# Kernel optimization log

Hardware: AMD Instinct MI355X
Metric: run time of the kernel (lower is better)

## Reference

```python
import jax, jax.numpy as jnp
import numpy as np

N = 50000
E = 1600000
IN_CH = 128
OUT_CH = 128
NEG_SLOPE = 0.2


def _gat_conv(x, W, att_src, att_dst, bias, src, dst, heads, out_ch, concat):
    # x: [N, F_in], W: [F_in, heads*out_ch], att_*: [heads, out_ch]
    n = x.shape[0]
    h = (x @ W).reshape(n, heads, out_ch)                    # [N, H, C]
    a_src = jnp.einsum('nhc,hc->nh', h, att_src)             # [N, H]
    a_dst = jnp.einsum('nhc,hc->nh', h, att_dst)             # [N, H]
    logits = jax.nn.leaky_relu(a_src[src] + a_dst[dst], NEG_SLOPE)  # [Etot, H]
    m = jax.ops.segment_max(logits, dst, num_segments=n)     # per-dst max (self-loops ensure non-empty)
    e = jnp.exp(logits - m[dst])
    denom = jax.ops.segment_sum(e, dst, num_segments=n)
    alpha = e / denom[dst]                                   # [Etot, H]
    msgs = h[src] * alpha[:, :, None]                        # [Etot, H, C]
    out = jax.ops.segment_sum(msgs, dst, num_segments=n)     # [N, H, C]
    out = out.reshape(n, heads * out_ch) if concat else out.mean(axis=1)
    return out + bias


def setup_inputs() -> dict:
    key = jax.random.key(0)
    ks = jax.random.split(key, 12)
    x = jax.random.normal(ks[0], (N, IN_CH), dtype=jnp.float32)
    edge_index = jax.random.randint(ks[1], (2, E), 0, N, dtype=jnp.int32)
    s = 0.1
    W_map = jax.random.normal(ks[2], (IN_CH, OUT_CH), dtype=jnp.float32) * s
    b_map = jnp.zeros((OUT_CH,), dtype=jnp.float32)
    # conv1: 128 -> 8 per head, 8 heads
    W1 = jax.random.normal(ks[3], (OUT_CH, 64), dtype=jnp.float32) * s
    att_src1 = jax.random.normal(ks[4], (8, 8), dtype=jnp.float32) * s
    att_dst1 = jax.random.normal(ks[5], (8, 8), dtype=jnp.float32) * s
    b1 = jnp.zeros((64,), dtype=jnp.float32)
    # conv2: 64 -> 128, 1 head, concat=False
    W2 = jax.random.normal(ks[6], (64, OUT_CH), dtype=jnp.float32) * s
    att_src2 = jax.random.normal(ks[7], (1, OUT_CH), dtype=jnp.float32) * s
    att_dst2 = jax.random.normal(ks[8], (1, OUT_CH), dtype=jnp.float32) * s
    b2 = jnp.zeros((OUT_CH,), dtype=jnp.float32)
    return {"x": x, "edge_index": edge_index, "W_map": W_map, "b_map": b_map,
            "W1": W1, "att_src1": att_src1, "att_dst1": att_dst1, "b1": b1,
            "W2": W2, "att_src2": att_src2, "att_dst2": att_dst2, "b2": b2}


def reference(x, edge_index, W_map, b_map, W1, att_src1, att_dst1, b1,
              W2, att_src2, att_dst2, b2):
    # add self-loops (PyG GATConv default)
    loops = jnp.arange(N, dtype=edge_index.dtype)
    src = jnp.concatenate([edge_index[0], loops])
    dst = jnp.concatenate([edge_index[1], loops])
    h = x @ W_map + b_map                                   # feature_mapping (dropout inactive in eval)
    h = _gat_conv(h, W1, att_src1, att_dst1, b1, src, dst, heads=8, out_ch=8, concat=True)
    h = jax.nn.elu(h)
    out = _gat_conv(h, W2, att_src2, att_dst2, b2, src, dst, heads=1, out_ch=OUT_CH, concat=False)
    return out
```

## Files before the change

### kernel.cpp

```cpp
#include <hip/hip_runtime.h>
#include <cstdint>
#include <cstddef>

#define NEG_SLOPE 0.2f
#define NBIN_MAX 1024
#define CAP_T 2560

typedef __attribute__((ext_vector_type(8))) short bf16x8;
typedef __attribute__((ext_vector_type(4))) float f32x4;

__device__ __forceinline__ float leaky(float x) { return x > 0.f ? x : NEG_SLOPE * x; }
__device__ __forceinline__ float blo(unsigned u) { return __uint_as_float(u << 16); }
__device__ __forceinline__ float bhi(unsigned u) { return __uint_as_float(u & 0xffff0000u); }
__device__ __forceinline__ unsigned short f2b(float f) {
    unsigned b = __float_as_uint(f);
    return (unsigned short)((b + 0x7fffu + ((b >> 16) & 1u)) >> 16);
}

__global__ void zero_i32(int* p, int n) {
    int i = blockIdx.x * 256 + threadIdx.x;
    if (i < n) p[i] = 0;
}

__global__ void prep_kernel(const float* __restrict__ Wm, const float* __restrict__ W1,
                            const float* __restrict__ bm, const float* __restrict__ W2,
                            unsigned short* __restrict__ WcT, float* __restrict__ bc,
                            unsigned short* __restrict__ W2T) {
    int t = blockIdx.x * 256 + threadIdx.x;
    if (t < 8192) {
        int n = t >> 7, k = t & 127;
        float acc = 0.f;
        for (int c = 0; c < 128; c++) acc = fmaf(Wm[k * 128 + c], W1[c * 64 + n], acc);
        WcT[n * 128 + k] = f2b(acc);
        if (t < 64) {
            float a = 0.f;
            for (int c = 0; c < 128; c++) a = fmaf(bm[c], W1[c * 64 + t], a);
            bc[t] = a;
        }
    } else if (t < 16384) {
        int u = t - 8192;
        int n = u >> 6, k = u & 63;
        W2T[n * 64 + k] = f2b(W2[k * 128 + n]);
    }
}

__global__ __launch_bounds__(256) void gemm1_mfma(
    const float* __restrict__ x, const unsigned short* __restrict__ WcT,
    const float* __restrict__ bc, unsigned short* __restrict__ h1b, int N) {
    int wave = threadIdx.x >> 6, l = threadIdx.x & 63;
    int mtile = blockIdx.x * 4 + wave;
    int mtiles = N >> 4;
    if (mtile >= mtiles) return;
    int lm = l & 15, quad = l >> 4;
    const float* xr = x + ((size_t)(mtile * 16 + lm)) * 128 + quad * 8;
    f32x4 acc[4];
#pragma unroll
    for (int nt = 0; nt < 4; nt++) acc[nt] = (f32x4){0.f, 0.f, 0.f, 0.f};
#pragma unroll
    for (int kk = 0; kk < 4; kk++) {
        float4 xa = ((const float4*)(xr + kk * 32))[0];
        float4 xb = ((const float4*)(xr + kk * 32 + 4))[0];
        bf16x8 a;
        a[0] = (short)f2b(xa.x); a[1] = (short)f2b(xa.y);
        a[2] = (short)f2b(xa.z); a[3] = (short)f2b(xa.w);
        a[4] = (short)f2b(xb.x); a[5] = (short)f2b(xb.y);
        a[6] = (short)f2b(xb.z); a[7] = (short)f2b(xb.w);
#pragma unroll
        for (int nt = 0; nt < 4; nt++) {
            bf16x8 b = *(const bf16x8*)(WcT + (nt * 16 + lm) * 128 + kk * 32 + quad * 8);
            acc[nt] = __builtin_amdgcn_mfma_f32_16x16x32_bf16(a, b, acc[nt], 0, 0, 0);
        }
    }
#pragma unroll
    for (int nt = 0; nt < 4; nt++) {
#pragma unroll
        for (int r = 0; r < 4; r++) {
            int row = mtile * 16 + quad * 4 + r;
            int col = nt * 16 + lm;
            h1b[(size_t)row * 64 + col] = f2b(acc[nt][r] + bc[col]);
        }
    }
}

__global__ __launch_bounds__(256) void att1_kernel(
    const unsigned* __restrict__ h1b, const float* __restrict__ att_s,
    const float* __restrict__ att_d, float* __restrict__ as1, float* __restrict__ ad1, int N) {
    __shared__ float ss[64], sd[64];
    if (threadIdx.x < 64) { ss[threadIdx.x] = att_s[threadIdx.x]; sd[threadIdx.x] = att_d[threadIdx.x]; }
    __syncthreads();
    int row = blockIdx.x * 256 + threadIdx.x;
    if (row >= N) return;
    const unsigned* hr = h1b + (size_t)row * 32;
#pragma unroll
    for (int h = 0; h < 8; h++) {
        float vs = 0.f, vd = 0.f;
#pragma unroll
        for (int cc = 0; cc < 4; cc++) {
            unsigned u = hr[h * 4 + cc];
            float lo = blo(u), hi = bhi(u);
            vs += lo * ss[h * 8 + 2 * cc] + hi * ss[h * 8 + 2 * cc + 1];
            vd += lo * sd[h * 8 + 2 * cc] + hi * sd[h * 8 + 2 * cc + 1];
        }
        as1[row * 8 + h] = vs;
        ad1[row * 8 + h] = vd;
    }
}

__global__ __launch_bounds__(256) void scatter2_kernel(
    const int* __restrict__ src, const int* __restrict__ dst, int E, int nbin,
    int* __restrict__ ccur, unsigned* __restrict__ tmp) {
    __shared__ int cnt[NBIN_MAX];
    for (int i = threadIdx.x; i < nbin; i += 256) cnt[i] = 0;
    __syncthreads();
    int chunk = (E + gridDim.x - 1) / gridDim.x;
    int beg = blockIdx.x * chunk;
    int end = beg + chunk; if (end > E) end = E;
    for (int i = beg + threadIdx.x; i < end; i += 256)
        atomicAdd(&cnt[dst[i] >> 6], 1);
    __syncthreads();
    for (int i = threadIdx.x; i < nbin; i += 256) {
        int c = cnt[i];
        cnt[i] = c ? atomicAdd(&ccur[i], c) : 0;
    }
    __syncthreads();
    for (int i = beg + threadIdx.x; i < end; i += 256) {
        int d = dst[i];
        int bin = d >> 6;
        int p = atomicAdd(&cnt[bin], 1);
        if (p < CAP_T)
            tmp[(size_t)bin * CAP_T + p] = ((unsigned)src[i] << 6) | (unsigned)(d & 63);
    }
}

__global__ __launch_bounds__(256) void bin_finalize(
    const unsigned* __restrict__ tmp, const int* __restrict__ ccur,
    int* __restrict__ off, int* __restrict__ degv,
    unsigned short* __restrict__ bucket, int N) {
    __shared__ int cnt[64];
    __shared__ int cur[64];
    int tid = threadIdx.x, b = blockIdx.x;
    if (tid < 64) cnt[tid] = 0;
    __syncthreads();
    int ecnt = ccur[b]; if (ecnt > CAP_T) ecnt = CAP_T;
    const unsigned* t = tmp + (size_t)b * CAP_T;
    for (int i = tid; i < ecnt; i += 256)
        atomicAdd(&cnt[t[i] & 63u], 1);
    __syncthreads();
    if (tid < 64) {
        int v = cnt[tid];
        int incl = v;
#pragma unroll
        for (int s = 1; s < 64; s <<= 1) {
            int u = __shfl_up(incl, s);
            if (tid >= s) incl += u;
        }
        int base = b * CAP_T + (incl - v);
        int node = b * 64 + tid;
        if (node < N) { off[node] = base; degv[node] = v; }
        cur[tid] = base;
    }
    __syncthreads();
    for (int i = tid; i < ecnt; i += 256) {
        unsigned u = t[i];
        int p = atomicAdd(&cur[u & 63u], 1);
        bucket[p] = (unsigned short)(u >> 6);
    }
}

__global__ __launch_bounds__(256) void conv1_agg(
    const int* __restrict__ off, const int* __restrict__ degv,
    const unsigned short* __restrict__ bucket,
    const unsigned* __restrict__ h1b, const float* __restrict__ as1,
    const float* __restrict__ ad1, const float* __restrict__ b1,
    unsigned* __restrict__ h1act, int N) {
    __shared__ uint2 lw[4][32][8];
    int wave = threadIdx.x >> 6, l = threadIdx.x & 63;
    int n = blockIdx.x * 4 + wave;
    if (n >= N) return;
    int begin = off[n];
    int deg = degv[n];
    int h = l & 7, eslot = l >> 3;
    float adst_h = ad1[n * 8 + h];
    float wself_h = __expf(leaky(as1[n * 8 + h] + adst_h));
    int c = l & 31, hp = c >> 2, half = l >> 5;
    float wself_c = __shfl(wself_h, hp);
    float acc0 = 0.f, acc1 = 0.f;
    if (half == 0) {
        unsigned u = h1b[(size_t)n * 32 + c];
        acc0 = wself_c * blo(u);
        acc1 = wself_c * bhi(u);
    }
    float den_l = 0.f;
    for (int c0 = 0; c0 < deg; c0 += 32) {
#pragma unroll
        for (int k = 0; k < 4; k++) {
            int e = eslot + 8 * k;
            int j = c0 + e;
            float w = 0.f; unsigned s = 0;
            if (j < deg) {
                s = bucket[begin + j];
                w = __expf(leaky(as1[s * 8 + h] + adst_h));
            }
            den_l += w;
            lw[wave][e][h] = make_uint2(__float_as_uint(w), s);
        }
        int cend = deg - c0; if (cend > 32) cend = 32;
        int e = half;
        for (; e + 14 < cend; e += 16) {
            float w[8]; unsigned s[8], u[8];
#pragma unroll
            for (int k = 0; k < 8; k++) {
                uint2 p = lw[wave][e + 2 * k][hp];
                w[k] = __uint_as_float(p.x); s[k] = p.y;
            }
#pragma unroll
            for (int k = 0; k < 8; k++) u[k] = h1b[(size_t)s[k] * 32 + c];
#pragma unroll
            for (int k = 0; k < 8; k++) {
                acc0 = fmaf(w[k], blo(u[k]), acc0);
                acc1 = fmaf(w[k], bhi(u[k]), acc1);
            }
        }
        for (; e < cend; e += 2) {
            uint2 p = lw[wave][e][hp];
            unsigned u = h1b[(size_t)p.y * 32 + c];
            float w = __uint_as_float(p.x);
            acc0 = fmaf(w, blo(u), acc0);
            acc1 = fmaf(w, bhi(u), acc1);
        }
    }
    den_l += __shfl_xor(den_l, 8);
    den_l += __shfl_xor(den_l, 16);
    den_l += __shfl_xor(den_l, 32);
    float den_full = den_l + wself_h;
    float den_c = __shfl(den_full, hp);
    acc0 += __shfl_xor(acc0, 32);
    acc1 += __shfl_xor(acc1, 32);
    if (half == 0) {
        float inv = 1.f / den_c;
        float2 bb = ((const float2*)b1)[c];
        float o0 = acc0 * inv + bb.x;
        float o1 = acc1 * inv + bb.y;
        o0 = o0 > 0.f ? o0 : __expf(o0) - 1.f;
        o1 = o1 > 0.f ? o1 : __expf(o1) - 1.f;
        h1act[(size_t)n * 32 + c] = (unsigned)f2b(o0) | ((unsigned)f2b(o1) << 16);
    }
}

__global__ __launch_bounds__(256) void gemm2_mfma(
    const unsigned short* __restrict__ h1act, const unsigned short* __restrict__ W2T,
    unsigned short* __restrict__ h2b, int N) {
    int wave = threadIdx.x >> 6, l = threadIdx.x & 63;
    int mtile = blockIdx.x * 4 + wave;
    int mtiles = N >> 4;
    if (mtile >= mtiles) return;
    int lm = l & 15, quad = l >> 4;
    const unsigned short* ar = h1act + (size_t)(mtile * 16 + lm) * 64 + quad * 8;
    bf16x8 a0 = *(const bf16x8*)(ar);
    bf16x8 a1 = *(const bf16x8*)(ar + 32);
    f32x4 acc[8];
#pragma unroll
    for (int nt = 0; nt < 8; nt++) acc[nt] = (f32x4){0.f, 0.f, 0.f, 0.f};
#pragma unroll
    for (int nt = 0; nt < 8; nt++) {
        const unsigned short* br = W2T + (nt * 16 + lm) * 64 + quad * 8;
        bf16x8 b0 = *(const bf16x8*)(br);
        bf16x8 b1v = *(const bf16x8*)(br + 32);
        acc[nt] = __builtin_amdgcn_mfma_f32_16x16x32_bf16(a0, b0, acc[nt], 0, 0, 0);
        acc[nt] = __builtin_amdgcn_mfma_f32_16x16x32_bf16(a1, b1v, acc[nt], 0, 0, 0);
    }
#pragma unroll
    for (int nt = 0; nt < 8; nt++) {
#pragma unroll
        for (int r = 0; r < 4; r++) {
            int row = mtile * 16 + quad * 4 + r;
            int col = nt * 16 + lm;
            h2b[(size_t)row * 128 + col] = f2b(acc[nt][r]);
        }
    }
}

__global__ __launch_bounds__(256) void att2_kernel(
    const unsigned* __restrict__ h2b, const float* __restrict__ att_s,
    const float* __restrict__ att_d, float* __restrict__ as2, float* __restrict__ ad2, int N) {
    __shared__ float ss[128], sd[128];
    if (threadIdx.x < 128) { ss[threadIdx.x] = att_s[threadIdx.x]; sd[threadIdx.x] = att_d[threadIdx.x]; }
    __syncthreads();
    int row = blockIdx.x * 256 + threadIdx.x;
    if (row >= N) return;
    const unsigned* hr = h2b + (size_t)row * 64;
    float vs = 0.f, vd = 0.f;
#pragma unroll 8
    for (int cc = 0; cc < 64; cc++) {
        unsigned u = hr[cc];
        float lo = blo(u), hi = bhi(u);
        vs += lo * ss[2 * cc] + hi * ss[2 * cc + 1];
        vd += lo * sd[2 * cc] + hi * sd[2 * cc + 1];
    }
    as2[row] = vs;
    ad2[row] = vd;
}

__global__ __launch_bounds__(256) void conv2_agg(
    const int* __restrict__ off, const int* __restrict__ degv,
    const unsigned short* __restrict__ bucket,
    const unsigned* __restrict__ h2b, const float* __restrict__ as2,
    const float* __restrict__ ad2, const float* __restrict__ b2,
    float* __restrict__ out, int N) {
    __shared__ uint2 ew[4][64];
    int wave = threadIdx.x >> 6, l = threadIdx.x & 63;
    int n = blockIdx.x * 4 + wave;
    if (n >= N) return;
    int begin = off[n];
    int deg = degv[n];
    float adst = ad2[n];
    float wself = __expf(leaky(as2[n] + adst));
    unsigned us = h2b[(size_t)n * 64 + l];
    float acc0 = wself * blo(us);
    float acc1 = wself * bhi(us);
    float den_l = 0.f;
    for (int c0 = 0; c0 < deg; c0 += 64) {
        int j = c0 + l;
        float w = 0.f; unsigned s = 0;
        if (j < deg) {
            s = bucket[begin + j];
            w = __expf(leaky(as2[s] + adst));
        }
        den_l += w;
        ew[wave][l] = make_uint2(__float_as_uint(w), s);
        int cend = deg - c0; if (cend > 64) cend = 64;
        int jj = 0;
        for (; jj + 8 <= cend; jj += 8) {
            float w[8]; unsigned s8[8], u[8];
#pragma unroll
            for (int k = 0; k < 8; k++) {
                uint2 p = ew[wave][jj + k];
                w[k] = __uint_as_float(p.x); s8[k] = p.y;
            }
#pragma unroll
            for (int k = 0; k < 8; k++) u[k] = h2b[(size_t)s8[k] * 64 + l];
#pragma unroll
            for (int k = 0; k < 8; k++) {
                acc0 = fmaf(w[k], blo(u[k]), acc0);
                acc1 = fmaf(w[k], bhi(u[k]), acc1);
            }
        }
        for (; jj < cend; jj++) {
            uint2 p0 = ew[wave][jj];
            unsigned u0 = h2b[(size_t)p0.y * 64 + l];
            float w0 = __uint_as_float(p0.x);
            acc0 = fmaf(w0, blo(u0), acc0); acc1 = fmaf(w0, bhi(u0), acc1);
        }
    }
#pragma unroll
    for (int s = 1; s < 64; s <<= 1) den_l += __shfl_xor(den_l, s);
    float inv = 1.f / (den_l + wself);
    float2 bb = ((const float2*)b2)[l];
    ((float2*)out)[(size_t)n * 64 + l] =
        make_float2(acc0 * inv + bb.x, acc1 * inv + bb.y);
}

extern "C" void kernel_launch(void* const* d_in, const int* in_sizes, int n_in,
                              void* d_out, int out_size, void* d_ws, size_t ws_size,
                              hipStream_t stream) {
    const float* x   = (const float*)d_in[0];
    const int*   ei  = (const int*)d_in[1];
    const float* Wm  = (const float*)d_in[2];
    const float* bm  = (const float*)d_in[3];
    const float* W1  = (const float*)d_in[4];
    const float* As1 = (const float*)d_in[5];
    const float* Ad1 = (const float*)d_in[6];
    const float* b1  = (const float*)d_in[7];
    const float* W2  = (const float*)d_in[8];
    const float* As2 = (const float*)d_in[9];
    const float* Ad2 = (const float*)d_in[10];
    const float* b2  = (const float*)d_in[11];
    int N = in_sizes[0] / 128;
    int E = in_sizes[1] / 2;
    const int* srcv = ei;
    const int* dstv = ei + E;

    char* p = (char*)d_ws;
    auto alloc = [&](size_t bytes) {
        void* r = (void*)p;
        p += (bytes + 255) & ~(size_t)255;
        return r;
    };
    int nbin = (N + 63) / 64;
    int*   degv   = (int*)alloc((size_t)N * 4);
    int*   off    = (int*)alloc((size_t)N * 4);
    int*   ccur   = (int*)alloc((size_t)nbin * 4);
    unsigned short* bucket = (unsigned short*)alloc((size_t)nbin * CAP_T * 2);
    unsigned short* WcT  = (unsigned short*)alloc(64 * 128 * 2);
    float*          bc   = (float*)alloc(64 * 4);
    unsigned short* W2T  = (unsigned short*)alloc(128 * 64 * 2);
    unsigned short* h1b  = (unsigned short*)alloc((size_t)N * 64 * 2);
    float* a_s1   = (float*)alloc((size_t)N * 8 * 4);
    float* a_d1   = (float*)alloc((size_t)N * 8 * 4);
    unsigned* h1act = (unsigned*)alloc((size_t)N * 64 * 2);
    unsigned short* h2b = (unsigned short*)alloc((size_t)N * 128 * 2);
    unsigned* tmp = (unsigned*)h2b;
    float* a_s2   = (float*)alloc((size_t)N * 4);
    float* a_d2   = (float*)alloc((size_t)N * 4);
    float* outp   = (float*)d_out;

    zero_i32<<<(nbin + 255) / 256, 256, 0, stream>>>(ccur, nbin);
    prep_kernel<<<64, 256, 0, stream>>>(Wm, W1, bm, W2, WcT, bc, W2T);
    scatter2_kernel<<<256, 256, 0, stream>>>(srcv, dstv, E, nbin, ccur, tmp);
    gemm1_mfma<<<(N / 16 + 3) / 4, 256, 0, stream>>>(x, WcT, bc, h1b, N);
    att1_kernel<<<(N + 255) / 256, 256, 0, stream>>>((const unsigned*)h1b, As1, Ad1, a_s1, a_d1, N);
    bin_finalize<<<nbin, 256, 0, stream>>>(tmp, ccur, off, degv, bucket, N);
    conv1_agg<<<(N + 3) / 4, 256, 0, stream>>>(off, degv, bucket, (const unsigned*)h1b, a_s1, a_d1, b1, h1act, N);
    gemm2_mfma<<<(N / 16 + 3) / 4, 256, 0, stream>>>((const unsigned short*)h1act, W2T, h2b, N);
    att2_kernel<<<(N + 255) / 256, 256, 0, stream>>>((const unsigned*)h2b, As2, Ad2, a_s2, a_d2, N);
    conv2_agg<<<(N + 3) / 4, 256, 0, stream>>>(off, degv, bucket, (const unsigned*)h2b, a_s2, a_d2, b2, outp, N);
}
```

Measured before the change: 285.7 us.

## Fuse attention-score dot products into GEMM epilogues and vectorize edge binning loads

The per-node attention coefficient kernels for both GAT layers are folded into the MFMA GEMM epilogues. Each lane multiplies its fp32 accumulator by the attention vector and the partial sums are reduced across lanes with shuffles, so the separate passes that reread h1/h2 from memory go away. The edge scatter kernel now reads src/dst as int4 with a scalar tail, and the zeroing kernel is replaced by hipMemsetAsync. Attention scores now come from fp32 values before bf16 rounding, which changes numerics slightly, and the extra shuffles lengthen the GEMM epilogue.

```diff
diff --git a/kernel.cpp b/kernel.cpp
--- a/kernel.cpp
+++ b/kernel.cpp
@@ -15,11 +15,6 @@
 __device__ __forceinline__ unsigned short f2b(float f) {
     unsigned b = __float_as_uint(f);
     return (unsigned short)((b + 0x7fffu + ((b >> 16) & 1u)) >> 16);
-}
-
-__global__ void zero_i32(int* p, int n) {
-    int i = blockIdx.x * 256 + threadIdx.x;
-    if (i < n) p[i] = 0;
 }
 
 __global__ void prep_kernel(const float* __restrict__ Wm, const float* __restrict__ W1,
@@ -46,7 +41,9 @@
 
 __global__ __launch_bounds__(256) void gemm1_mfma(
     const float* __restrict__ x, const unsigned short* __restrict__ WcT,
-    const float* __restrict__ bc, unsigned short* __restrict__ h1b, int N) {
+    const float* __restrict__ bc, const float* __restrict__ att_s,
+    const float* __restrict__ att_d, unsigned short* __restrict__ h1b,
+    float* __restrict__ as1, float* __restrict__ ad1, int N) {
     int wave = threadIdx.x >> 6, l = threadIdx.x & 63;
     int mtile = blockIdx.x * 4 + wave;
     int mtiles = N >> 4;
@@ -71,38 +68,41 @@
             acc[nt] = __builtin_amdgcn_mfma_f32_16x16x32_bf16(a, b, acc[nt], 0, 0, 0);
         }
     }
+    float vs[4][4], vd[4][4];
 #pragma unroll
     for (int nt = 0; nt < 4; nt++) {
+        int col = nt * 16 + lm;
+        float sA = att_s[col], dA = att_d[col], bcv = bc[col];
 #pragma unroll
         for (int r = 0; r < 4; r++) {
+            float hv = acc[nt][r] + bcv;
             int row = mtile * 16 + quad * 4 + r;
-            int col = nt * 16 + lm;
-            h1b[(size_t)row * 64 + col] = f2b(acc[nt][r] + bc[col]);
-        }
-    }
-}
-
-__global__ __launch_bounds__(256) void att1_kernel(
-    const unsigned* __restrict__ h1b, const float* __restrict__ att_s,
-    const float* __restrict__ att_d, float* __restrict__ as1, float* __restrict__ ad1, int N) {
-    __shared__ float ss[64], sd[64];
-    if (threadIdx.x < 64) { ss[threadIdx.x] = att_s[threadIdx.x]; sd[threadIdx.x] = att_d[threadIdx.x]; }
-    __syncthreads();
-    int row = blockIdx.x * 256 + threadIdx.x;
-    if (row >= N) return;
-    const unsigned* hr = h1b + (size_t)row * 32;
-#pragma unroll
-    for (int h = 0; h < 8; h++) {
-        float vs = 0.f, vd = 0.f;
-#pragma unroll
-        for (int cc = 0; cc < 4; cc++) {
-            unsigned u = hr[h * 4 + cc];
-            float lo = blo(u), hi = bhi(u);
-            vs += lo * ss[h * 8 + 2 * cc] + hi * ss[h * 8 + 2 * cc + 1];
-            vd += lo * sd[h * 8 + 2 * cc] + hi * sd[h * 8 + 2 * cc + 1];
-        }
-        as1[row * 8 + h] = vs;
-        ad1[row * 8 + h] = vd;
+            h1b[(size_t)row * 64 + col] = f2b(hv);
+            vs[nt][r] = hv * sA;
+            vd[nt][r] = hv * dA;
+        }
+    }
+#pragma unroll
+    for (int m = 1; m < 8; m <<= 1)
+#pragma unroll
+        for (int nt = 0; nt < 4; nt++)
+#pragma unroll
+            for (int r = 0; r < 4; r++) {
+                vs[nt][r] += __shfl_xor(vs[nt][r], m);
+                vd[nt][r] += __shfl_xor(vd[nt][r], m);
+            }
+    if ((lm & 7) == 0) {
+        int hbase = lm >> 3;
+#pragma unroll
+        for (int nt = 0; nt < 4; nt++) {
+            int H = 2 * nt + hbase;
+#pragma unroll
+            for (int r = 0; r < 4; r++) {
+                int row = mtile * 16 + quad * 4 + r;
+                as1[row * 8 + H] = vs[nt][r];
+                ad1[row * 8 + H] = vd[nt][r];
+            }
+        }
     }
 }
 
@@ -112,24 +112,50 @@
     __shared__ int cnt[NBIN_MAX];
     for (int i = threadIdx.x; i < nbin; i += 256) cnt[i] = 0;
     __syncthreads();
-    int chunk = (E + gridDim.x - 1) / gridDim.x;
-    int beg = blockIdx.x * chunk;
-    int end = beg + chunk; if (end > E) end = E;
-    for (int i = beg + threadIdx.x; i < end; i += 256)
-        atomicAdd(&cnt[dst[i] >> 6], 1);
+    int E4 = E >> 2;
+    int chunk4 = (E4 + gridDim.x - 1) / gridDim.x;
+    int b4 = blockIdx.x * chunk4;
+    int e4 = b4 + chunk4; if (e4 > E4) e4 = E4;
+    const int4* dst4 = (const int4*)dst;
+    const int4* src4 = (const int4*)src;
+    bool last = (blockIdx.x == gridDim.x - 1);
+    for (int i = b4 + threadIdx.x; i < e4; i += 256) {
+        int4 d = dst4[i];
+        atomicAdd(&cnt[d.x >> 6], 1);
+        atomicAdd(&cnt[d.y >> 6], 1);
+        atomicAdd(&cnt[d.z >> 6], 1);
+        atomicAdd(&cnt[d.w >> 6], 1);
+    }
+    if (last)
+        for (int i = (E4 << 2) + threadIdx.x; i < E; i += 256)
+            atomicAdd(&cnt[dst[i] >> 6], 1);
     __syncthreads();
     for (int i = threadIdx.x; i < nbin; i += 256) {
         int c = cnt[i];
         cnt[i] = c ? atomicAdd(&ccur[i], c) : 0;
     }
     __syncthreads();
-    for (int i = beg + threadIdx.x; i < end; i += 256) {
-        int d = dst[i];
-        int bin = d >> 6;
-        int p = atomicAdd(&cnt[bin], 1);
-        if (p < CAP_T)
-            tmp[(size_t)bin * CAP_T + p] = ((unsigned)src[i] << 6) | (unsigned)(d & 63);
-    }
+    for (int i = b4 + threadIdx.x; i < e4; i += 256) {
+        int4 d = dst4[i];
+        int4 s = src4[i];
+#pragma unroll
+        for (int k = 0; k < 4; k++) {
+            int dd = (k == 0) ? d.x : (k == 1) ? d.y : (k == 2) ? d.z : d.w;
+            int ss = (k == 0) ? s.x : (k == 1) ? s.y : (k == 2) ? s.z : s.w;
+            int bin = dd >> 6;
+            int p = atomicAdd(&cnt[bin], 1);
+            if (p < CAP_T)
+                tmp[(size_t)bin * CAP_T + p] = ((unsigned)ss << 6) | (unsigned)(dd & 63);
+        }
+    }
+    if (last)
+        for (int i = (E4 << 2) + threadIdx.x; i < E; i += 256) {
+            int dd = dst[i];
+            int bin = dd >> 6;
+            int p = atomicAdd(&cnt[bin], 1);
+            if (p < CAP_T)
+                tmp[(size_t)bin * CAP_T + p] = ((unsigned)src[i] << 6) | (unsigned)(dd & 63);
+        }
 }
 
 __global__ __launch_bounds__(256) void bin_finalize(
@@ -249,7 +275,9 @@
 
 __global__ __launch_bounds__(256) void gemm2_mfma(
     const unsigned short* __restrict__ h1act, const unsigned short* __restrict__ W2T,
-    unsigned short* __restrict__ h2b, int N) {
+    const float* __restrict__ att_s2, const float* __restrict__ att_d2,
+    unsigned short* __restrict__ h2b, float* __restrict__ as2, float* __restrict__ ad2,
+    int N) {
     int wave = threadIdx.x >> 6, l = threadIdx.x & 63;
     int mtile = blockIdx.x * 4 + wave;
     int mtiles = N >> 4;
@@ -269,36 +297,35 @@
         acc[nt] = __builtin_amdgcn_mfma_f32_16x16x32_bf16(a0, b0, acc[nt], 0, 0, 0);
         acc[nt] = __builtin_amdgcn_mfma_f32_16x16x32_bf16(a1, b1v, acc[nt], 0, 0, 0);
     }
+    float vs[4] = {0.f, 0.f, 0.f, 0.f}, vd[4] = {0.f, 0.f, 0.f, 0.f};
 #pragma unroll
     for (int nt = 0; nt < 8; nt++) {
+        int col = nt * 16 + lm;
+        float sA = att_s2[col], dA = att_d2[col];
+#pragma unroll
+        for (int r = 0; r < 4; r++) {
+            float hv = acc[nt][r];
+            int row = mtile * 16 + quad * 4 + r;
+            h2b[(size_t)row * 128 + col] = f2b(hv);
+            vs[r] = fmaf(hv, sA, vs[r]);
+            vd[r] = fmaf(hv, dA, vd[r]);
+        }
+    }
+#pragma unroll
+    for (int m = 1; m < 16; m <<= 1)
+#pragma unroll
+        for (int r = 0; r < 4; r++) {
+            vs[r] += __shfl_xor(vs[r], m);
+            vd[r] += __shfl_xor(vd[r], m);
+        }
+    if (lm == 0) {
 #pragma unroll
         for (int r = 0; r < 4; r++) {
             int row = mtile * 16 + quad * 4 + r;
-            int col = nt * 16 + lm;
-            h2b[(size_t)row * 128 + col] = f2b(acc[nt][r]);
-        }
-    }
-}
-
-__global__ __launch_bounds__(256) void att2_kernel(
-    const unsigned* __restrict__ h2b, const float* __restrict__ att_s,
-    const float* __restrict__ att_d, float* __restrict__ as2, float* __restrict__ ad2, int N) {
-    __shared__ float ss[128], sd[128];
-    if (threadIdx.x < 128) { ss[threadIdx.x] = att_s[threadIdx.x]; sd[threadIdx.x] = att_d[threadIdx.x]; }
-    __syncthreads();
-    int row = blockIdx.x * 256 + threadIdx.x;
-    if (row >= N) return;
-    const unsigned* hr = h2b + (size_t)row * 64;
-    float vs = 0.f, vd = 0.f;
-#pragma unroll 8
-    for (int cc = 0; cc < 64; cc++) {
-        unsigned u = hr[cc];
-        float lo = blo(u), hi = bhi(u);
-        vs += lo * ss[2 * cc] + hi * ss[2 * cc + 1];
-        vd += lo * sd[2 * cc] + hi * sd[2 * cc + 1];
-    }
-    as2[row] = vs;
-    ad2[row] = vd;
+            as2[row] = vs[r];
+            ad2[row] = vd[r];
+        }
+    }
 }
 
 __global__ __launch_bounds__(256) void conv2_agg(
@@ -404,14 +431,12 @@
     float* a_d2   = (float*)alloc((size_t)N * 4);
     float* outp   = (float*)d_out;
 
-    zero_i32<<<(nbin + 255) / 256, 256, 0, stream>>>(ccur, nbin);
+    hipMemsetAsync(ccur, 0, (size_t)nbin * 4, stream);
     prep_kernel<<<64, 256, 0, stream>>>(Wm, W1, bm, W2, WcT, bc, W2T);
     scatter2_kernel<<<256, 256, 0, stream>>>(srcv, dstv, E, nbin, ccur, tmp);
-    gemm1_mfma<<<(N / 16 + 3) / 4, 256, 0, stream>>>(x, WcT, bc, h1b, N);
-    att1_kernel<<<(N + 255) / 256, 256, 0, stream>>>((const unsigned*)h1b, As1, Ad1, a_s1, a_d1, N);
+    gemm1_mfma<<<(N / 16 + 3) / 4, 256, 0, stream>>>(x, WcT, bc, As1, Ad1, h1b, a_s1, a_d1, N);
     bin_finalize<<<nbin, 256, 0, stream>>>(tmp, ccur, off, degv, bucket, N);
     conv1_agg<<<(N + 3) / 4, 256, 0, stream>>>(off, degv, bucket, (const unsigned*)h1b, a_s1, a_d1, b1, h1act, N);
-    gemm2_mfma<<<(N / 16 + 3) / 4, 256, 0, stream>>>((const unsigned short*)h1act, W2T, h2b, N);
-    att2_kernel<<<(N + 255) / 256, 256, 0, stream>>>((const unsigned*)h2b, As2, Ad2, a_s2, a_d2, N);
+    gemm2_mfma<<<(N / 16 + 3) / 4, 256, 0, stream>>>((const unsigned short*)h1act, W2T, As2, Ad2, h2b, a_s2, a_d2, N);
     conv2_agg<<<(N + 3) / 4, 256, 0, stream>>>(off, degv, bucket, (const unsigned*)h2b, a_s2, a_d2, b2, outp, N);
 }
```

Result: faster. 269.6 us (-5.6%).
